# Optimization experiments

Measured on AMD Instinct MI355X. Metric: run time of the kernel, lower is better.

The kernel has to match this reference:

```python
import jax, jax.numpy as jnp
import numpy as np

B, S, E, H, DH, F = 4, 2048, 1024, 4, 256, 4096


def setup_inputs() -> dict:
    key = jax.random.key(0)
    ks = jax.random.split(key, 16)
    def w(k, shape):
        return jax.random.normal(k, shape, jnp.float32) * 0.02
    return {
        "inputs": jax.random.normal(ks[0], (B, S, E), jnp.float32),
        "context": jax.random.normal(ks[1], (B, S, E), jnp.float32),
        # self-attention (causal) per-head projections stacked over heads
        "Wk1": w(ks[2], (H, E, DH)), "bk1": jnp.zeros((H, DH), jnp.float32),
        "Wq1": w(ks[3], (H, E, DH)), "bq1": jnp.zeros((H, DH), jnp.float32),
        "Wv1": w(ks[4], (H, E, DH)), "bv1": jnp.zeros((H, DH), jnp.float32),
        "Wo1": w(ks[5], (E, E)), "bo1": jnp.zeros((E,), jnp.float32),
        # cross-attention (no mask)
        "Wk2": w(ks[6], (H, E, DH)), "bk2": jnp.zeros((H, DH), jnp.float32),
        "Wq2": w(ks[7], (H, E, DH)), "bq2": jnp.zeros((H, DH), jnp.float32),
        "Wv2": w(ks[8], (H, E, DH)), "bv2": jnp.zeros((H, DH), jnp.float32),
        "Wo2": w(ks[9], (E, E)), "bo2": jnp.zeros((E,), jnp.float32),
        "ln_g": jnp.ones((E,), jnp.float32), "ln_b": jnp.zeros((E,), jnp.float32),
        # FFN
        "W1": w(ks[10], (E, F)), "b1": jnp.zeros((F,), jnp.float32),
        "W2": w(ks[11], (F, E)), "b2": jnp.zeros((E,), jnp.float32),
    }


def _mha(kin, vin, qin, Wk, bk, Wq, bq, Wv, bv, Wo, bo, causal):
    # per-head Dense projections, batched over heads: [B,S,E] x [H,E,DH] -> [B,H,S,DH]
    K = jnp.einsum('bse,hed->bhsd', kin, Wk) + bk[None, :, None, :]
    Q = jnp.einsum('bse,hed->bhsd', qin, Wq) + bq[None, :, None, :]
    V = jnp.einsum('bse,hed->bhsd', vin, Wv) + bv[None, :, None, :]
    # NOTE: original divides by head_dim (K.get_shape()[2]), NOT sqrt(head_dim)
    scores = jnp.einsum('bhqd,bhkd->bhqk', Q, K) / K.shape[-1]
    if causal:
        sq, sk = scores.shape[-2], scores.shape[-1]
        mask = jnp.triu(jnp.full((sq, sk), -jnp.inf, scores.dtype), k=1)
        scores = scores + mask  # additive -inf strictly above the diagonal
    A = jax.nn.softmax(scores, axis=-1)
    # concat heads in order along the feature axis, then output Dense
    out = jnp.einsum('bhqk,bhkd->bqhd', A, V).reshape(qin.shape[0], qin.shape[1], -1)
    return out @ Wo + bo


def _ln(x, g, b):
    # keras LayerNormalization default epsilon = 1e-3
    m = x.mean(-1, keepdims=True)
    v = ((x - m) ** 2).mean(-1, keepdims=True)
    return (x - m) / jnp.sqrt(v + 1e-3) * g + b


def reference(inputs, context, Wk1, bk1, Wq1, bq1, Wv1, bv1, Wo1, bo1,
              Wk2, bk2, Wq2, bq2, Wv2, bv2, Wo2, bo2,
              ln_g, ln_b, W1, b1, W2, b2):
    # dropout layers are identity at inference
    a = _mha(inputs, inputs, inputs, Wk1, bk1, Wq1, bq1, Wv1, bv1, Wo1, bo1, True) + inputs
    a = _ln(a, ln_g, ln_b)
    # cross-attention: keys/values = context, queries = normalized self-attn output
    c = _mha(context, context, a, Wk2, bk2, Wq2, bq2, Wv2, bv2, Wo2, bo2, False) + a
    c = _ln(c, ln_g, ln_b)
    h = jax.nn.relu(c @ W1 + b1) @ W2 + b2 + c
    return jax.nn.relu(_ln(h, ln_g, ln_b))
```

## Files before the change

kernel.cpp:

```cpp
#include <hip/hip_runtime.h>

#define DEV __device__ __forceinline__

typedef unsigned short u16;
typedef __bf16 bf16x8 __attribute__((ext_vector_type(8)));
typedef bf16x8 __attribute__((may_alias)) bf16x8a;
typedef float f32x4 __attribute__((ext_vector_type(4)));
typedef float f32x16 __attribute__((ext_vector_type(16)));

constexpr int NB = 4, NS = 2048, NE = 1024, NH = 4, NDH = 256, NF = 4096;
constexpr int NR = NB * NS;

DEV u16 f2bf(float f) {
  unsigned u = __float_as_uint(f);
  u += 0x7fff + ((u >> 16) & 1);
  return (u16)(u >> 16);
}

DEV f32x4 mfma16(bf16x8 a, bf16x8 b, f32x4 c) {
  return __builtin_amdgcn_mfma_f32_16x16x32_bf16(a, b, c, 0, 0, 0);
}
DEV f32x16 mfma32(bf16x8 a, bf16x8 b, f32x16 c) {
  return __builtin_amdgcn_mfma_f32_32x32x16_bf16(a, b, c, 0, 0, 0);
}

DEV bf16x8 ldfrag(const u16* p) { return *(const bf16x8a*)p; }

DEV void gload_lds16(const void* g, void* l) {
  __builtin_amdgcn_global_load_lds(
      (const __attribute__((address_space(1))) void*)g,
      (__attribute__((address_space(3))) void*)l, 16, 0, 0);
}

DEV void blockbar() {
  asm volatile("" ::: "memory");
  __builtin_amdgcn_s_barrier();
  asm volatile("" ::: "memory");
}

DEV unsigned packbf(float a, float b) {
  union { __bf16 h[2]; unsigned u; } x;
  x.h[0] = (__bf16)a; x.h[1] = (__bf16)b;
  return x.u;
}

__global__ void cast_f32_bf16(const float* __restrict__ in, u16* __restrict__ out, int n4) {
  int i = blockIdx.x * 256 + threadIdx.x;
  if (i >= n4) return;
  float4 v = ((const float4*)in)[i];
  ushort4 o;
  o.x = f2bf(v.x); o.y = f2bf(v.y); o.z = f2bf(v.z); o.w = f2bf(v.w);
  ((ushort4*)out)[i] = o;
}

__global__ void transpose_cast(const float* __restrict__ in, u16* __restrict__ out, int R, int C) {
  __shared__ float t[32][33];
  size_t base = (size_t)blockIdx.z * R * C;
  int c0 = blockIdx.x * 32, r0 = blockIdx.y * 32;
  int x = threadIdx.x;
  for (int yy = threadIdx.y; yy < 32; yy += 8)
    t[yy][x] = in[base + (size_t)(r0 + yy) * C + c0 + x];
  __syncthreads();
  for (int yy = threadIdx.y; yy < 32; yy += 8)
    out[base + (size_t)(c0 + yy) * R + r0 + x] = f2bf(t[x][yy]);
}

__global__ void transpose_v(const u16* __restrict__ V, int vstride, u16* __restrict__ Vt) {
  __shared__ u16 t[32][34];
  int bh = blockIdx.z, b = bh >> 2, h = bh & (NH - 1);
  int s0 = blockIdx.x * 32, d0 = blockIdx.y * 32;
  int x = threadIdx.x;
  for (int yy = threadIdx.y; yy < 32; yy += 8)
    t[yy][x] = V[(size_t)(b * NS + s0 + yy) * vstride + h * NDH + d0 + x];
  __syncthreads();
  for (int yy = threadIdx.y; yy < 32; yy += 8)
    Vt[((size_t)bh * NDH + d0 + yy) * NS + s0 + x] = t[x][yy];
}

__global__ void copy_f32(const float* __restrict__ s, float* __restrict__ d, int n) {
  int i = blockIdx.x * 256 + threadIdx.x;
  if (i < n) d[i] = s[i];
}

template<int OUTF32, int RELU>
__global__ __launch_bounds__(256, 2)
void gemm_bt(const u16* __restrict__ A, const u16* __restrict__ Bt,
             const float* __restrict__ bias, const float* __restrict__ res,
             float* __restrict__ outF, u16* __restrict__ outB,
             int M, int N, int K)
{
  __shared__ u16 lA[128 * 32];
  __shared__ u16 lB[128 * 32];
  int tid = threadIdx.x;
  int wid = tid >> 6, lane = tid & 63;
  int lr = lane & 15, lk = lane >> 4;
  int wm = wid >> 1, wn = wid & 1;

  int flat = blockIdx.y * gridDim.x + blockIdx.x;
  int cpx = (gridDim.x * gridDim.y) >> 3;
  int swz = (flat & 7) * cpx + (flat >> 3);
  int bx = swz % gridDim.x, by = swz / gridDim.x;
  int rowBlk = by * 128, colBlk = bx * 128;

  f32x4 acc[4][4];
#pragma unroll
  for (int i = 0; i < 4; i++)
#pragma unroll
    for (int j = 0; j < 4; j++) acc[i][j] = (f32x4){0.f, 0.f, 0.f, 0.f};

  const u16* gA = A + (size_t)(rowBlk + wid * 32 + (lane >> 2)) * K + (lane & 3) * 8;
  const u16* gB = Bt + (size_t)(colBlk + wid * 32 + (lane >> 2)) * K + (lane & 3) * 8;
  u16* lAw = lA + wid * 1024;
  u16* lBw = lB + wid * 1024;

  for (int kk = 0; kk < K; kk += 32) {
    __syncthreads();
    gload_lds16(gA + kk, lAw);
    gload_lds16(gA + kk + (size_t)16 * K, lAw + 512);
    gload_lds16(gB + kk, lBw);
    gload_lds16(gB + kk + (size_t)16 * K, lBw + 512);
    asm volatile("s_waitcnt vmcnt(0)" ::: "memory");
    __syncthreads();

    bf16x8 af[4], bf[4];
#pragma unroll
    for (int fm = 0; fm < 4; fm++)
      af[fm] = ldfrag(lA + (wm * 64 + fm * 16 + lr) * 32 + lk * 8);
#pragma unroll
    for (int fn = 0; fn < 4; fn++)
      bf[fn] = ldfrag(lB + (wn * 64 + fn * 16 + lr) * 32 + lk * 8);
#pragma unroll
    for (int fm = 0; fm < 4; fm++)
#pragma unroll
      for (int fn = 0; fn < 4; fn++)
        acc[fm][fn] = mfma16(af[fm], bf[fn], acc[fm][fn]);
  }

  int orow = rowBlk + wm * 64;
  int ocol = colBlk + wn * 64;
#pragma unroll
  for (int fn = 0; fn < 4; fn++) {
    int c = ocol + fn * 16 + lr;
    float bv = bias[c];
#pragma unroll
    for (int fm = 0; fm < 4; fm++) {
      int r0 = orow + fm * 16 + lk * 4;
#pragma unroll
      for (int j = 0; j < 4; j++) {
        float v = acc[fm][fn][j] + bv;
        if (OUTF32) v += res[(size_t)(r0 + j) * N + c];
        if (RELU) v = fmaxf(v, 0.f);
        if (OUTF32) outF[(size_t)(r0 + j) * N + c] = v;
        else        outB[(size_t)(r0 + j) * N + c] = f2bf(v);
      }
    }
  }
}

template<int CAUSAL>
__global__ __launch_bounds__(512, 2)
void attn8w(const u16* __restrict__ Qp, int qstride,
            const u16* __restrict__ Kp, int kstride,
            const u16* __restrict__ Vt, u16* __restrict__ O)
{
  __shared__ __align__(16) u16 smem[65536];

  int bidx = blockIdx.x;
  int bh = bidx & 15;
  int qt = CAUSAL ? (15 - (bidx >> 4)) : (bidx >> 4);
  int b = bh >> 2, h = bh & 3;
  int tid = threadIdx.x, w = tid >> 6, lane = tid & 63;
  int L = lane & 31, hi = lane >> 5;
  int g = w >> 1, ks = w & 1;

  int qbase = qt * 128 + g * 32;

  const u16* qrow = Qp + (size_t)(b * NS + qbase + L) * qstride + h * NDH;
  bf16x8 qf[16];
#pragma unroll
  for (int s = 0; s < 16; s++) qf[s] = ldfrag(qrow + s * 16 + hi * 8);

  f32x16 oacc[8];
#pragma unroll
  for (int db = 0; db < 8; db++) oacc[db] = (f32x16){};
  float m = -1e30f, l = 0.f;

  int nkt = CAUSAL ? (2 * qt + 2) : (NS / 64);
  constexpr float SC = 1.0f / NDH;

  const u16* kbase = Kp + (size_t)(b * NS) * kstride + h * NDH;
  const u16* vbase = Vt + (size_t)bh * NDH * NS;

  auto stage = [&](int kt, int buf) {
#pragma unroll
    for (int ii = 0; ii < 4; ii++) {
      int gi = w * 4 + ii;
      int krow = 2 * gi + hi;
      int kcol = L ^ (krow & 31);
      gload_lds16(kbase + (size_t)(kt * 64 + krow) * kstride + kcol * 8,
                  &smem[buf * 16384 + gi * 512]);
      int vd = gi * 8 + (lane >> 3);
      int vg = (lane & 7) ^ (vd & 7);
      gload_lds16(vbase + (size_t)vd * NS + kt * 64 + vg * 8,
                  &smem[32768 + buf * 16384 + gi * 512]);
    }
  };

  stage(0, 0);

  for (int kt = 0; kt < nkt; kt++) {
    int buf = kt & 1;
    const u16* bK = &smem[buf * 16384];
    const u16* bV = &smem[32768 + buf * 16384];
    if (kt + 1 < nkt) {
      stage(kt + 1, buf ^ 1);
      asm volatile("s_waitcnt vmcnt(8)" ::: "memory");
    } else {
      asm volatile("s_waitcnt vmcnt(0)" ::: "memory");
    }
    blockbar();

    int ksub0 = kt * 64 + ks * 32;
    bool skip = CAUSAL && (ksub0 > qbase + 31);
    if (!skip) {
      bool domask = CAUSAL && (ksub0 + 31 > qbase);
      __builtin_amdgcn_s_setprio(1);
      f32x16 sa = (f32x16){};
#pragma unroll
      for (int s = 0; s < 16; s++) {
        int row = ks * 32 + L;
        bf16x8 kf = ldfrag(&bK[row * 256 + (((2 * s + hi) ^ L) & 31) * 8]);
        sa = mfma32(kf, qf[s], sa);
      }
      __builtin_amdgcn_s_setprio(0);

      float p[16];
      float tmax = -1e30f;
#pragma unroll
      for (int r = 0; r < 16; r++) {
        float v = sa[r] * SC;
        if (domask) {
          int key = ksub0 + (r & 3) + 8 * (r >> 2) + 4 * hi;
          if (key > qbase + L) v = -1e30f;
        }
        p[r] = v;
        tmax = fmaxf(tmax, v);
      }
      tmax = fmaxf(tmax, __shfl_xor(tmax, 32));

      float mn = m;
      if (!__all(tmax - m <= 5.0f)) {
        mn = fmaxf(m, tmax);
        float rs = __expf(m - mn);
        m = mn;
        l *= rs;
#pragma unroll
        for (int db = 0; db < 8; db++)
#pragma unroll
          for (int r = 0; r < 16; r++) oacc[db][r] *= rs;
      }
      float psum = 0.f;
#pragma unroll
      for (int r = 0; r < 16; r++) {
        p[r] = __expf(p[r] - mn);
        psum += p[r];
      }
      psum += __shfl_xor(psum, 32);
      l += psum;

      unsigned pk01 = packbf(p[0], p[1]),  pk23 = packbf(p[2], p[3]);
      unsigned pk45 = packbf(p[4], p[5]),  pk67 = packbf(p[6], p[7]);
      unsigned pk89 = packbf(p[8], p[9]),  pkab = packbf(p[10], p[11]);
      unsigned pkcd = packbf(p[12], p[13]), pkef = packbf(p[14], p[15]);
      unsigned s45 = (unsigned)__shfl_xor((int)pk45, 32);
      unsigned s67 = (unsigned)__shfl_xor((int)pk67, 32);
      unsigned s01 = (unsigned)__shfl_xor((int)pk01, 32);
      unsigned s23 = (unsigned)__shfl_xor((int)pk23, 32);
      unsigned scd = (unsigned)__shfl_xor((int)pkcd, 32);
      unsigned sef = (unsigned)__shfl_xor((int)pkef, 32);
      unsigned s89 = (unsigned)__shfl_xor((int)pk89, 32);
      unsigned sab = (unsigned)__shfl_xor((int)pkab, 32);
      union { unsigned u[4]; bf16x8 v; } fb0, fb1;
      fb0.u[0] = hi ? s45 : pk01;
      fb0.u[1] = hi ? s67 : pk23;
      fb0.u[2] = hi ? pk45 : s01;
      fb0.u[3] = hi ? pk67 : s23;
      fb1.u[0] = hi ? scd : pk89;
      fb1.u[1] = hi ? sef : pkab;
      fb1.u[2] = hi ? pkcd : s89;
      fb1.u[3] = hi ? pkef : sab;
      bf16x8 pb0 = fb0.v, pb1 = fb1.v;

      __builtin_amdgcn_s_setprio(1);
#pragma unroll
      for (int db = 0; db < 8; db++) {
        int vd = db * 32 + L;
        bf16x8 vf0 = ldfrag(&bV[vd * 64 + (((ks * 4 + hi) ^ (vd & 7)) & 7) * 8]);
        bf16x8 vf1 = ldfrag(&bV[vd * 64 + (((ks * 4 + 2 + hi) ^ (vd & 7)) & 7) * 8]);
        oacc[db] = mfma32(vf0, pb0, oacc[db]);
        oacc[db] = mfma32(vf1, pb1, oacc[db]);
      }
      __builtin_amdgcn_s_setprio(0);
    }
    blockbar();
  }

  float* fsm = (float*)smem;
  blockbar();
  if (hi == 0) { fsm[w * 64 + L * 2] = m; fsm[w * 64 + L * 2 + 1] = l; }
  blockbar();
  float mb = fsm[(w ^ 1) * 64 + L * 2];
  float lb = fsm[(w ^ 1) * 64 + L * 2 + 1];
  float M = fmaxf(m, mb);
  float eo = __expf(m - M);
  float lt = l * eo + lb * __expf(mb - M);
  blockbar();
  float* reg = fsm + g * 8192;
  if (w & 1) {
#pragma unroll
    for (int db = 0; db < 8; db++)
#pragma unroll
      for (int r = 0; r < 16; r++) {
        int d = db * 32 + (r & 3) + 8 * (r >> 2) + 4 * hi;
        reg[d * 32 + L] = oacc[db][r] * eo;
      }
  }
  blockbar();
  if (!(w & 1)) {
    float inv = 1.f / lt;
    size_t orow = (size_t)(b * NS + qbase + L) * NE + h * NDH;
#pragma unroll
    for (int db = 0; db < 8; db++) {
#pragma unroll
      for (int rq = 0; rq < 4; rq++) {
        int d0 = db * 32 + rq * 8 + hi * 4;
        float a0 = (oacc[db][rq * 4 + 0] * eo + reg[(d0 + 0) * 32 + L]) * inv;
        float a1 = (oacc[db][rq * 4 + 1] * eo + reg[(d0 + 1) * 32 + L]) * inv;
        float a2 = (oacc[db][rq * 4 + 2] * eo + reg[(d0 + 2) * 32 + L]) * inv;
        float a3 = (oacc[db][rq * 4 + 3] * eo + reg[(d0 + 3) * 32 + L]) * inv;
        uint2 wv;
        wv.x = packbf(a0, a1);
        wv.y = packbf(a2, a3);
        *(uint2*)&O[orow + d0] = wv;
      }
    }
  }
}

template<int RELU, int WBF>
__global__ __launch_bounds__(256)
void ln_kernel(const float* __restrict__ x, const float* __restrict__ g,
               const float* __restrict__ bb, float* __restrict__ outF,
               u16* __restrict__ outB)
{
  int row = blockIdx.x, tid = threadIdx.x;
  float4 v = ((const float4*)(x + (size_t)row * NE))[tid];
  float s = v.x + v.y + v.z + v.w;
  float s2 = v.x * v.x + v.y * v.y + v.z * v.z + v.w * v.w;
#pragma unroll
  for (int off = 32; off; off >>= 1) {
    s += __shfl_xor(s, off);
    s2 += __shfl_xor(s2, off);
  }
  __shared__ float red[8];
  int wid = tid >> 6, lane = tid & 63;
  if (lane == 0) { red[wid] = s; red[4 + wid] = s2; }
  __syncthreads();
  s = red[0] + red[1] + red[2] + red[3];
  s2 = red[4] + red[5] + red[6] + red[7];
  float mean = s * (1.f / NE);
  float var = s2 * (1.f / NE) - mean * mean;
  float rstd = rsqrtf(var + 1e-3f);
  float4 gg = ((const float4*)g)[tid];
  float4 bv = ((const float4*)bb)[tid];
  float4 o;
  o.x = (v.x - mean) * rstd * gg.x + bv.x;
  o.y = (v.y - mean) * rstd * gg.y + bv.y;
  o.z = (v.z - mean) * rstd * gg.z + bv.z;
  o.w = (v.w - mean) * rstd * gg.w + bv.w;
  if (RELU) {
    o.x = fmaxf(o.x, 0.f); o.y = fmaxf(o.y, 0.f);
    o.z = fmaxf(o.z, 0.f); o.w = fmaxf(o.w, 0.f);
  }
  ((float4*)(outF + (size_t)row * NE))[tid] = o;
  if (WBF) {
    ushort4 ob;
    ob.x = f2bf(o.x); ob.y = f2bf(o.y); ob.z = f2bf(o.z); ob.w = f2bf(o.w);
    ((ushort4*)(outB + (size_t)row * NE))[tid] = ob;
  }
}

constexpr size_t OFF_X    = 0;
constexpr size_t OFF_W    = OFF_X + 16777216;
constexpr size_t OFF_BIAS = OFF_W + 33554432;
constexpr size_t OFF_QKV  = OFF_BIAS + 32768;
constexpr size_t OFF_VT   = OFF_QKV + 50331648;
constexpr size_t OFF_T0   = OFF_VT + 16777216;
constexpr size_t OFF_A    = OFF_T0 + 33554432;
constexpr size_t OFF_ABF  = OFF_A + 33554432;

extern "C" void kernel_launch(void* const* d_in, const int* in_sizes, int n_in,
                              void* d_out, int out_size, void* d_ws, size_t ws_size,
                              hipStream_t stream) {
  (void)in_sizes; (void)n_in; (void)out_size; (void)ws_size;
  const float* inp = (const float*)d_in[0];
  const float* ctx = (const float*)d_in[1];
  const float* Wk1 = (const float*)d_in[2];  const float* bk1 = (const float*)d_in[3];
  const float* Wq1 = (const float*)d_in[4];  const float* bq1 = (const float*)d_in[5];
  const float* Wv1 = (const float*)d_in[6];  const float* bv1 = (const float*)d_in[7];
  const float* Wo1 = (const float*)d_in[8];  const float* bo1 = (const float*)d_in[9];
  const float* Wk2 = (const float*)d_in[10]; const float* bk2 = (const float*)d_in[11];
  const float* Wq2 = (const float*)d_in[12]; const float* bq2 = (const float*)d_in[13];
  const float* Wv2 = (const float*)d_in[14]; const float* bv2 = (const float*)d_in[15];
  const float* Wo2 = (const float*)d_in[16]; const float* bo2 = (const float*)d_in[17];
  const float* lng = (const float*)d_in[18]; const float* lnb = (const float*)d_in[19];
  const float* W1  = (const float*)d_in[20]; const float* b1  = (const float*)d_in[21];
  const float* W2  = (const float*)d_in[22]; const float* b2  = (const float*)d_in[23];
  float* out = (float*)d_out;
  char* ws = (char*)d_ws;

  u16* XBF    = (u16*)(ws + OFF_X);
  u16* WQKV1T = (u16*)(ws + OFF_W);
  u16* WKV2T  = WQKV1T + 3072 * 1024;
  u16* WQ2T   = WKV2T + 2048 * 1024;
  u16* WO1T   = WQ2T + 1024 * 1024;
  u16* WO2T   = WO1T + 1024 * 1024;
  u16* W1T    = WO2T + 1024 * 1024;
  u16* W2T    = W1T + 4096 * 1024;
  float* BQKV1 = (float*)(ws + OFF_BIAS);
  float* BKV2  = BQKV1 + 3072;
  u16* QKV  = (u16*)(ws + OFF_QKV);
  u16* Q2   = QKV + 8192 * 2048;
  u16* VT   = (u16*)(ws + OFF_VT);
  u16* MID  = QKV;
  float* T0 = (float*)(ws + OFF_T0);
  float* Af = (float*)(ws + OFF_A);
  u16* ABF  = (u16*)(ws + OFF_ABF);
  u16* Obuf = XBF;

  dim3 tb(32, 8);

  cast_f32_bf16<<<8192, 256, 0, stream>>>(inp, XBF, NR * NE / 4);
  transpose_cast<<<dim3(8, 32, 4), tb, 0, stream>>>(Wk1, WQKV1T,               NE, NDH);
  transpose_cast<<<dim3(8, 32, 4), tb, 0, stream>>>(Wq1, WQKV1T + 1024 * 1024, NE, NDH);
  transpose_cast<<<dim3(8, 32, 4), tb, 0, stream>>>(Wv1, WQKV1T + 2048 * 1024, NE, NDH);
  transpose_cast<<<dim3(32, 32, 1), tb, 0, stream>>>(Wo1, WO1T, NE, NE);
  transpose_cast<<<dim3(8, 32, 4), tb, 0, stream>>>(Wk2, WKV2T,               NE, NDH);
  transpose_cast<<<dim3(8, 32, 4), tb, 0, stream>>>(Wv2, WKV2T + 1024 * 1024, NE, NDH);
  transpose_cast<<<dim3(8, 32, 4), tb, 0, stream>>>(Wq2, WQ2T, NE, NDH);
  transpose_cast<<<dim3(32, 32, 1), tb, 0, stream>>>(Wo2, WO2T, NE, NE);
  transpose_cast<<<dim3(128, 32, 1), tb, 0, stream>>>(W1, W1T, NE, NF);
  transpose_cast<<<dim3(32, 128, 1), tb, 0, stream>>>(W2, W2T, NF, NE);
  copy_f32<<<4, 256, 0, stream>>>(bk1, BQKV1, 1024);
  copy_f32<<<4, 256, 0, stream>>>(bq1, BQKV1 + 1024, 1024);
  copy_f32<<<4, 256, 0, stream>>>(bv1, BQKV1 + 2048, 1024);
  copy_f32<<<4, 256, 0, stream>>>(bk2, BKV2, 1024);
  copy_f32<<<4, 256, 0, stream>>>(bv2, BKV2 + 1024, 1024);

  gemm_bt<0, 0><<<dim3(24, 64), 256, 0, stream>>>(XBF, WQKV1T, BQKV1, nullptr,
                                                  nullptr, QKV, NR, 3072, NE);
  transpose_v<<<dim3(64, 8, 16), tb, 0, stream>>>(QKV + 2048, 3072, VT);
  attn8w<1><<<256, 512, 0, stream>>>(QKV + 1024, 3072, QKV, 3072, VT, Obuf);
  gemm_bt<1, 0><<<dim3(8, 64), 256, 0, stream>>>(Obuf, WO1T, bo1, inp,
                                                 T0, nullptr, NR, NE, NE);
  ln_kernel<0, 1><<<NR, 256, 0, stream>>>(T0, lng, lnb, Af, ABF);

  cast_f32_bf16<<<8192, 256, 0, stream>>>(ctx, XBF, NR * NE / 4);
  gemm_bt<0, 0><<<dim3(16, 64), 256, 0, stream>>>(XBF, WKV2T, BKV2, nullptr,
                                                  nullptr, QKV, NR, 2048, NE);
  gemm_bt<0, 0><<<dim3(8, 64), 256, 0, stream>>>(ABF, WQ2T, bq2, nullptr,
                                                 nullptr, Q2, NR, NE, NE);
  transpose_v<<<dim3(64, 8, 16), tb, 0, stream>>>(QKV + 1024, 2048, VT);
  attn8w<0><<<256, 512, 0, stream>>>(Q2, 1024, QKV, 2048, VT, Obuf);
  gemm_bt<1, 0><<<dim3(8, 64), 256, 0, stream>>>(Obuf, WO2T, bo2, Af,
                                                 T0, nullptr, NR, NE, NE);
  ln_kernel<0, 1><<<NR, 256, 0, stream>>>(T0, lng, lnb, Af, ABF);

  gemm_bt<0, 1><<<dim3(32, 64), 256, 0, stream>>>(ABF, W1T, b1, nullptr,
                                                  nullptr, MID, NR, NF, NE);
  gemm_bt<1, 0><<<dim3(8, 64), 256, 0, stream>>>(MID, W2T, b2, Af,
                                                 T0, nullptr, NR, NE, NF);
  ln_kernel<1, 0><<<NR, 256, 0, stream>>>(T0, lng, lnb, out, nullptr);
}
```

Before: 789.1 us.

## Replace GEMM with 8-wave 256-row double-buffered swizzled-LDS kernel

Replaces the 128x128 single-buffered GEMM with an 8-wave kernel using 256xBN tiles, K-step 64, double-buffered LDS with XOR-swizzled layout, and prefetch of the next K tile interleaved with MFMA phases. The goal is to hide global-load latency, raise data reuse per block and cut LDS bank conflicts. In exchange there are fewer blocks (occupancy 1), more register pressure from the larger accumulators, and tail quantisation for the N=1024 GEMMs with fewer tiles.

```diff
diff --git a/kernel.cpp b/kernel.cpp
--- a/kernel.cpp
+++ b/kernel.cpp
@@ -82,72 +82,127 @@
   if (i < n) d[i] = s[i];
 }
 
-template<int OUTF32, int RELU>
-__global__ __launch_bounds__(256, 2)
-void gemm_bt(const u16* __restrict__ A, const u16* __restrict__ Bt,
-             const float* __restrict__ bias, const float* __restrict__ res,
-             float* __restrict__ outF, u16* __restrict__ outB,
-             int M, int N, int K)
+template<int BN, int OUTF32, int RELU>
+__global__ __launch_bounds__(512, 1)
+void gemm8p(const u16* __restrict__ A, const u16* __restrict__ Bt,
+            const float* __restrict__ bias, const float* __restrict__ res,
+            float* __restrict__ outF, u16* __restrict__ outB,
+            int M, int N, int K)
 {
-  __shared__ u16 lA[128 * 32];
-  __shared__ u16 lB[128 * 32];
-  int tid = threadIdx.x;
-  int wid = tid >> 6, lane = tid & 63;
+  constexpr int NFRAG = BN / 64;
+  __shared__ __align__(16) u16 smem[32768 + 2 * BN * 64];
+
+  int tid = threadIdx.x, w = tid >> 6, lane = tid & 63;
   int lr = lane & 15, lk = lane >> 4;
-  int wm = wid >> 1, wn = wid & 1;
+  int wm = w >> 2, wn = w & 3;
 
   int flat = blockIdx.y * gridDim.x + blockIdx.x;
   int cpx = (gridDim.x * gridDim.y) >> 3;
   int swz = (flat & 7) * cpx + (flat >> 3);
   int bx = swz % gridDim.x, by = swz / gridDim.x;
-  int rowBlk = by * 128, colBlk = bx * 128;
-
-  f32x4 acc[4][4];
-#pragma unroll
-  for (int i = 0; i < 4; i++)
-#pragma unroll
-    for (int j = 0; j < 4; j++) acc[i][j] = (f32x4){0.f, 0.f, 0.f, 0.f};
-
-  const u16* gA = A + (size_t)(rowBlk + wid * 32 + (lane >> 2)) * K + (lane & 3) * 8;
-  const u16* gB = Bt + (size_t)(colBlk + wid * 32 + (lane >> 2)) * K + (lane & 3) * 8;
-  u16* lAw = lA + wid * 1024;
-  u16* lBw = lB + wid * 1024;
-
-  for (int kk = 0; kk < K; kk += 32) {
-    __syncthreads();
-    gload_lds16(gA + kk, lAw);
-    gload_lds16(gA + kk + (size_t)16 * K, lAw + 512);
-    gload_lds16(gB + kk, lBw);
-    gload_lds16(gB + kk + (size_t)16 * K, lBw + 512);
-    asm volatile("s_waitcnt vmcnt(0)" ::: "memory");
-    __syncthreads();
-
-    bf16x8 af[4], bf[4];
-#pragma unroll
-    for (int fm = 0; fm < 4; fm++)
-      af[fm] = ldfrag(lA + (wm * 64 + fm * 16 + lr) * 32 + lk * 8);
-#pragma unroll
-    for (int fn = 0; fn < 4; fn++)
-      bf[fn] = ldfrag(lB + (wn * 64 + fn * 16 + lr) * 32 + lk * 8);
-#pragma unroll
-    for (int fm = 0; fm < 4; fm++)
-#pragma unroll
-      for (int fn = 0; fn < 4; fn++)
-        acc[fm][fn] = mfma16(af[fm], bf[fn], acc[fm][fn]);
-  }
-
-  int orow = rowBlk + wm * 64;
-  int ocol = colBlk + wn * 64;
-#pragma unroll
-  for (int fn = 0; fn < 4; fn++) {
-    int c = ocol + fn * 16 + lr;
+  int rowBlk = by * 256, colBlk = bx * BN;
+
+  f32x4 acc[8][NFRAG];
+#pragma unroll
+  for (int f = 0; f < 8; f++)
+#pragma unroll
+    for (int n = 0; n < NFRAG; n++) acc[f][n] = (f32x4){0.f, 0.f, 0.f, 0.f};
+
+  int srow = lane >> 3;
+  int scol = ((lane & 7) ^ (srow & 7)) * 8;
+
+  const u16* gA = A + (size_t)rowBlk * K;
+  const u16* gB = Bt + (size_t)colBlk * K;
+
+  auto stageA = [&](int t, int p, int h) {
+#pragma unroll
+    for (int j = 0; j < 2; j++) {
+      int rbase = h * 128 + (w * 2 + j) * 8;
+      gload_lds16(gA + (size_t)(rbase + srow) * K + t * 64 + scol,
+                  &smem[(p * 256 + rbase) * 64]);
+    }
+  };
+  auto stageB = [&](int t, int p, int h) {
+#pragma unroll
+    for (int j = 0; j < 2; j++) {
+      int rbase = h * 128 + (w * 2 + j) * 8;
+      gload_lds16(gB + (size_t)(rbase + srow) * K + t * 64 + scol,
+                  &smem[32768 + (p * BN + rbase) * 64]);
+    }
+  };
+
+  stageB(0, 0, 0);
+  if (BN == 256) stageB(0, 0, 1);
+  stageA(0, 0, 0);
+  stageA(0, 0, 1);
+  asm volatile("s_waitcnt vmcnt(0)" ::: "memory");
+  blockbar();
+
+  int NT = K >> 6;
+  for (int t = 0; t < NT; t++) {
+    int p = t & 1;
+    bool pre = (t + 1 < NT);
+    bf16x8 bf[NFRAG][2];
+#pragma unroll
+    for (int q = 0; q < 4; q++) {
+      if (q == 0) {
+#pragma unroll
+        for (int n = 0; n < NFRAG; n++)
+#pragma unroll
+          for (int s = 0; s < 2; s++) {
+            int rowB = wn * (BN >> 2) + n * 16 + lr;
+            bf[n][s] = ldfrag(&smem[32768 + (p * BN + rowB) * 64 +
+                                    (((s * 4 + lk) ^ (lr & 7)) * 8)]);
+          }
+      }
+      bf16x8 af[2][2];
+#pragma unroll
+      for (int i = 0; i < 2; i++)
+#pragma unroll
+        for (int s = 0; s < 2; s++) {
+          int rowA = wm * 128 + (q * 2 + i) * 16 + lr;
+          af[i][s] = ldfrag(&smem[(p * 256 + rowA) * 64 +
+                                  (((s * 4 + lk) ^ (lr & 7)) * 8)]);
+        }
+      if (pre) {
+        if (BN == 256) {
+          if (q == 0) { stageB(t + 1, p ^ 1, 0); stageB(t + 1, p ^ 1, 1); }
+          else if (q == 1) stageA(t + 1, p ^ 1, 0);
+          else if (q == 2) stageA(t + 1, p ^ 1, 1);
+        } else {
+          if (q == 0) stageB(t + 1, p ^ 1, 0);
+          else if (q == 1) stageA(t + 1, p ^ 1, 0);
+          else if (q == 2) stageA(t + 1, p ^ 1, 1);
+        }
+      }
+      blockbar();
+      asm volatile("s_waitcnt lgkmcnt(0)" ::: "memory");
+      __builtin_amdgcn_s_setprio(1);
+#pragma unroll
+      for (int i = 0; i < 2; i++)
+#pragma unroll
+        for (int n = 0; n < NFRAG; n++)
+#pragma unroll
+          for (int s = 0; s < 2; s++)
+            acc[q * 2 + i][n] = mfma16(af[i][s], bf[n][s], acc[q * 2 + i][n]);
+      __builtin_amdgcn_s_setprio(0);
+      if (q == 3) asm volatile("s_waitcnt vmcnt(0)" ::: "memory");
+      blockbar();
+    }
+  }
+
+  int orow0 = rowBlk + wm * 128;
+  int ocol0 = colBlk + wn * (BN >> 2);
+#pragma unroll
+  for (int n = 0; n < NFRAG; n++) {
+    int c = ocol0 + n * 16 + lr;
     float bv = bias[c];
 #pragma unroll
-    for (int fm = 0; fm < 4; fm++) {
-      int r0 = orow + fm * 16 + lk * 4;
+    for (int f = 0; f < 8; f++) {
+      int r0 = orow0 + f * 16 + lk * 4;
 #pragma unroll
       for (int j = 0; j < 4; j++) {
-        float v = acc[fm][fn][j] + bv;
+        float v = acc[f][n][j] + bv;
         if (OUTF32) v += res[(size_t)(r0 + j) * N + c];
         if (RELU) v = fmaxf(v, 0.f);
         if (OUTF32) outF[(size_t)(r0 + j) * N + c] = v;
@@ -457,28 +512,28 @@
   copy_f32<<<4, 256, 0, stream>>>(bk2, BKV2, 1024);
   copy_f32<<<4, 256, 0, stream>>>(bv2, BKV2 + 1024, 1024);
 
-  gemm_bt<0, 0><<<dim3(24, 64), 256, 0, stream>>>(XBF, WQKV1T, BQKV1, nullptr,
-                                                  nullptr, QKV, NR, 3072, NE);
+  gemm8p<256, 0, 0><<<dim3(12, 32), 512, 0, stream>>>(XBF, WQKV1T, BQKV1, nullptr,
+                                                      nullptr, QKV, NR, 3072, NE);
   transpose_v<<<dim3(64, 8, 16), tb, 0, stream>>>(QKV + 2048, 3072, VT);
   attn8w<1><<<256, 512, 0, stream>>>(QKV + 1024, 3072, QKV, 3072, VT, Obuf);
-  gemm_bt<1, 0><<<dim3(8, 64), 256, 0, stream>>>(Obuf, WO1T, bo1, inp,
-                                                 T0, nullptr, NR, NE, NE);
+  gemm8p<128, 1, 0><<<dim3(8, 32), 512, 0, stream>>>(Obuf, WO1T, bo1, inp,
+                                                     T0, nullptr, NR, NE, NE);
   ln_kernel<0, 1><<<NR, 256, 0, stream>>>(T0, lng, lnb, Af, ABF);
 
   cast_f32_bf16<<<8192, 256, 0, stream>>>(ctx, XBF, NR * NE / 4);
-  gemm_bt<0, 0><<<dim3(16, 64), 256, 0, stream>>>(XBF, WKV2T, BKV2, nullptr,
-                                                  nullptr, QKV, NR, 2048, NE);
-  gemm_bt<0, 0><<<dim3(8, 64), 256, 0, stream>>>(ABF, WQ2T, bq2, nullptr,
-                                                 nullptr, Q2, NR, NE, NE);
+  gemm8p<256, 0, 0><<<dim3(8, 32), 512, 0, stream>>>(XBF, WKV2T, BKV2, nullptr,
+                                                     nullptr, QKV, NR, 2048, NE);
+  gemm8p<128, 0, 0><<<dim3(8, 32), 512, 0, stream>>>(ABF, WQ2T, bq2, nullptr,
+                                                     nullptr, Q2, NR, NE, NE);
   transpose_v<<<dim3(64, 8, 16), tb, 0, stream>>>(QKV + 1024, 2048, VT);
   attn8w<0><<<256, 512, 0, stream>>>(Q2, 1024, QKV, 2048, VT, Obuf);
-  gemm_bt<1, 0><<<dim3(8, 64), 256, 0, stream>>>(Obuf, WO2T, bo2, Af,
-                                                 T0, nullptr, NR, NE, NE);
+  gemm8p<128, 1, 0><<<dim3(8, 32), 512, 0, stream>>>(Obuf, WO2T, bo2, Af,
+                                                     T0, nullptr, NR, NE, NE);
   ln_kernel<0, 1><<<NR, 256, 0, stream>>>(T0, lng, lnb, Af, ABF);
 
-  gemm_bt<0, 1><<<dim3(32, 64), 256, 0, stream>>>(ABF, W1T, b1, nullptr,
-                                                  nullptr, MID, NR, NF, NE);
-  gemm_bt<1, 0><<<dim3(8, 64), 256, 0, stream>>>(MID, W2T, b2, Af,
-                                                 T0, nullptr, NR, NE, NF);
+  gemm8p<256, 0, 1><<<dim3(16, 32), 512, 0, stream>>>(ABF, W1T, b1, nullptr,
+                                                      nullptr, MID, NR, NF, NE);
+  gemm8p<128, 1, 0><<<dim3(8, 32), 512, 0, stream>>>(MID, W2T, b2, Af,
+                                                     T0, nullptr, NR, NE, NF);
   ln_kernel<1, 0><<<NR, 256, 0, stream>>>(T0, lng, lnb, out, nullptr);
 }
```

After: 744.9 us. -5.6%, faster.
